# Optimization experiments

Measured on AMD Instinct MI355X. Metric: run time of the kernel, lower is better.

Reference implementation:

```python
import jax, jax.numpy as jnp
import numpy as np

H, NH, NKV, HD, S, B = 4096, 32, 8, 128, 2048, 1
QMAX = 127.0  # int8 symmetric


def fake_quant(x, axis=None):
    """Symmetric int8 fake quantization with straight-through estimator.
    axis=None -> per-tensor dynamic scale; axis=int -> per-channel along that axis."""
    if axis is None:
        amax = jnp.max(jnp.abs(x))
    else:
        amax = jnp.max(jnp.abs(x), axis=axis, keepdims=True)
    scale = jnp.maximum(amax, 1e-8) / QMAX
    q = jnp.clip(jnp.round(x / scale), -QMAX - 1, QMAX) * scale
    return x + jax.lax.stop_gradient(q - x)


def quant_linear(x, w):
    # weight: per-output-channel quant (reduce over in-features axis=1);
    # activation: per-tensor dynamic quant
    xq = fake_quant(x)
    wq = fake_quant(w, axis=1)
    return jnp.einsum('bsh,oh->bso', xq, wq)


def rotate_half(x):
    x1, x2 = jnp.split(x, 2, axis=-1)
    return jnp.concatenate([-x2, x1], axis=-1)


def apply_rope(q, k, cos, sin):
    # q: [B,NH,S,HD], k: [B,NKV,S,HD], cos/sin: [B,S,HD]
    cos = cos[:, None, :, :]
    sin = sin[:, None, :, :]
    return q * cos + rotate_half(q) * sin, k * cos + rotate_half(k) * sin


def setup_inputs() -> dict:
    key = jax.random.key(0)
    ks = jax.random.split(key, 6)
    hidden_states = jax.random.normal(ks[0], (B, S, H), jnp.float32)
    # additive causal mask
    neg = jnp.finfo(jnp.float32).min
    mask = jnp.where(jnp.tril(jnp.ones((S, S), bool)), 0.0, neg)
    attention_mask = jnp.broadcast_to(mask, (B, 1, S, S)).astype(jnp.float32)
    # rotary cos/sin
    inv_freq = 1.0 / (10000.0 ** (jnp.arange(0, HD, 2, dtype=jnp.float32) / HD))
    t = jnp.arange(S, dtype=jnp.float32)
    freqs = jnp.outer(t, inv_freq)                     # [S, HD/2]
    emb = jnp.concatenate([freqs, freqs], axis=-1)     # [S, HD]
    cos = jnp.broadcast_to(jnp.cos(emb), (B, S, HD))
    sin = jnp.broadcast_to(jnp.sin(emb), (B, S, HD))
    sc = 0.02
    wq = jax.random.normal(ks[1], (H, H), jnp.float32) * sc
    wk = jax.random.normal(ks[2], (NKV * HD, H), jnp.float32) * sc
    wv = jax.random.normal(ks[3], (NKV * HD, H), jnp.float32) * sc
    wo = jax.random.normal(ks[4], (H, H), jnp.float32) * sc
    return {"hidden_states": hidden_states, "attention_mask": attention_mask,
            "cos": cos, "sin": sin, "wq": wq, "wk": wk, "wv": wv, "wo": wo}


def reference(hidden_states, attention_mask, cos, sin, wq, wk, wv, wo):
    b, s, _ = hidden_states.shape
    scaling = HD ** -0.5
    q = quant_linear(hidden_states, wq).reshape(b, s, NH, HD).transpose(0, 2, 1, 3)
    k = quant_linear(hidden_states, wk).reshape(b, s, NKV, HD).transpose(0, 2, 1, 3)
    v = quant_linear(hidden_states, wv).reshape(b, s, NKV, HD).transpose(0, 2, 1, 3)
    q, k = apply_rope(q, k, cos, sin)
    groups = NH // NKV
    k = jnp.repeat(k, groups, axis=1)  # [B,NH,S,HD]
    v = jnp.repeat(v, groups, axis=1)
    # quantize before QK^T
    qq = fake_quant(q)
    kq = fake_quant(k)
    attn = jnp.einsum('bhqd,bhkd->bhqk', qq, kq) * scaling
    attn = attn + attention_mask
    attn = jnp.maximum(attn, jnp.finfo(attn.dtype).min)
    attn = jax.nn.softmax(attn.astype(jnp.float32), axis=-1).astype(q.dtype)
    # quantize before PV
    pq = fake_quant(attn)
    vq = fake_quant(v)
    out = jnp.einsum('bhqk,bhkd->bhqd', pq, vq)
    out = out.transpose(0, 2, 1, 3).reshape(b, s, NH * HD)
    out = quant_linear(out, wo)
    return out
```

## Files before the change

kernel.cpp:

```cpp
#include <hip/hip_runtime.h>
#include <cstdint>
#include <cstddef>


#define S_LEN   2048
#define HDIM    4096
#define NHEADS  32
#define NKVH    8
#define HEADD   128
#define QMAXF   127.0f
#define ROPE_BLOCKS 20480

typedef _Float16 half8  __attribute__((ext_vector_type(8)));
typedef float    floatx4 __attribute__((ext_vector_type(4)));

__device__ __forceinline__ float wave_max64(float v){
#pragma unroll
  for (int off = 32; off > 0; off >>= 1) v = fmaxf(v, __shfl_xor(v, off));
  return v;
}
__device__ __forceinline__ float grp16_max(float v){
#pragma unroll
  for (int off = 8; off > 0; off >>= 1) v = fmaxf(v, __shfl_xor(v, off));
  return v;
}
__device__ __forceinline__ float grp16_sum(float v){
#pragma unroll
  for (int off = 8; off > 0; off >>= 1) v += __shfl_xor(v, off);
  return v;
}
__device__ __forceinline__ void atomic_max_f(unsigned* p, float v){
  atomicMax(p, __float_as_uint(v));
}
__device__ __forceinline__ float q8(float x, float scale){
  return fminf(fmaxf(rintf(x / scale), -128.f), 127.f);
}
__device__ __forceinline__ void gload_lds16(const _Float16* g, _Float16* l){
  __builtin_amdgcn_global_load_lds((const __attribute__((address_space(1))) void*)g,
                                   (__attribute__((address_space(3))) void*)l, 16, 0, 0);
}

__device__ __forceinline__ void block_atomic_max(float m, unsigned* out){
  m = wave_max64(m);
  __shared__ float red[4];
  int wid = threadIdx.x >> 6;
  if ((threadIdx.x & 63) == 0) red[wid] = m;
  __syncthreads();
  if (threadIdx.x == 0)
    atomic_max_f(out, fmaxf(fmaxf(red[0], red[1]), fmaxf(red[2], red[3])));
}

__global__ void k_init(float* scal){ if (threadIdx.x < 16) scal[threadIdx.x] = 0.0f; }

__global__ void k_amax(const float* __restrict__ x, size_t n4, unsigned* __restrict__ out){
  size_t i = (size_t)blockIdx.x * blockDim.x + threadIdx.x;
  size_t stride = (size_t)gridDim.x * blockDim.x;
  float m = 0.f;
  for (; i < n4; i += stride){
    float4 v = ((const float4*)x)[i];
    m = fmaxf(m, fmaxf(fmaxf(fabsf(v.x), fabsf(v.y)), fmaxf(fabsf(v.z), fabsf(v.w))));
  }
  block_atomic_max(m, out);
}

__global__ void k_amax_v(const float* __restrict__ Y, unsigned* __restrict__ out){
  size_t i = (size_t)blockIdx.x * blockDim.x + threadIdx.x;
  size_t stride = (size_t)gridDim.x * blockDim.x;
  float m = 0.f;
  for (size_t e = i; e < (size_t)S_LEN * 1024; e += stride){
    size_t s = e >> 10; int c = (int)(e & 1023);
    m = fmaxf(m, fabsf(Y[s * 6144 + 5120 + c]));
  }
  block_atomic_max(m, out);
}

__global__ void k_quant(const float* __restrict__ x, _Float16* __restrict__ q,
                        size_t n4, const float* __restrict__ amax){
  float scale = fmaxf(*amax, 1e-8f) / QMAXF;
  size_t i = (size_t)blockIdx.x * blockDim.x + threadIdx.x;
  size_t stride = (size_t)gridDim.x * blockDim.x;
  for (; i < n4; i += stride){
    float4 v = ((const float4*)x)[i];
    union { _Float16 h[4]; uint2 u; } pk;
    pk.h[0] = (_Float16)q8(v.x, scale);
    pk.h[1] = (_Float16)q8(v.y, scale);
    pk.h[2] = (_Float16)q8(v.z, scale);
    pk.h[3] = (_Float16)q8(v.w, scale);
    ((uint2*)q)[i] = pk.u;
  }
}

__global__ __launch_bounds__(256) void k_quant_w(
    const float* __restrict__ wq, const float* __restrict__ wk,
    const float* __restrict__ wv, const float* __restrict__ wo,
    _Float16* __restrict__ Wall, _Float16* __restrict__ Wo,
    float* __restrict__ wsc)
{
  int row = blockIdx.x;
  const float* src; _Float16* dst;
  if (row < 4096)      { src = wq + (size_t)row * HDIM;          dst = Wall + (size_t)row * HDIM; }
  else if (row < 5120) { src = wk + (size_t)(row - 4096) * HDIM; dst = Wall + (size_t)row * HDIM; }
  else if (row < 6144) { src = wv + (size_t)(row - 5120) * HDIM; dst = Wall + (size_t)row * HDIM; }
  else                 { src = wo + (size_t)(row - 6144) * HDIM; dst = Wo + (size_t)(row - 6144) * HDIM; }
  float4 v[4]; float m = 0.f;
#pragma unroll
  for (int i = 0; i < 4; i++){
    v[i] = ((const float4*)src)[threadIdx.x + i * 256];
    m = fmaxf(m, fmaxf(fmaxf(fabsf(v[i].x), fabsf(v[i].y)), fmaxf(fabsf(v[i].z), fabsf(v[i].w))));
  }
  m = wave_max64(m);
  __shared__ float red[4];
  int wid = threadIdx.x >> 6;
  if ((threadIdx.x & 63) == 0) red[wid] = m;
  __syncthreads();
  float am = fmaxf(fmaxf(red[0], red[1]), fmaxf(red[2], red[3]));
  float scale = fmaxf(am, 1e-8f) / QMAXF;
  if (threadIdx.x == 0) wsc[row] = scale;
#pragma unroll
  for (int i = 0; i < 4; i++){
    union { _Float16 h[4]; uint2 u; } pk;
    pk.h[0] = (_Float16)q8(v[i].x, scale);
    pk.h[1] = (_Float16)q8(v[i].y, scale);
    pk.h[2] = (_Float16)q8(v[i].z, scale);
    pk.h[3] = (_Float16)q8(v[i].w, scale);
    ((uint2*)dst)[threadIdx.x + i * 256] = pk.u;
  }
}

__global__ __launch_bounds__(256) void k_rope(
    float* __restrict__ Y, const float* __restrict__ cosb,
    const float* __restrict__ sinb,
    float* __restrict__ qpart, float* __restrict__ kpart)
{
  int idx = blockIdx.x * 256 + threadIdx.x;
  int s = idx / (40 * 64);
  int rem = idx - s * 40 * 64;
  int head = rem >> 6;
  int d = rem & 63;
  size_t base = (size_t)s * 6144 + (head < 32 ? head * 128 : 4096 + (head - 32) * 128);
  float x1 = Y[base + d], x2 = Y[base + d + 64];
  float c1 = cosb[s * 128 + d],      s1 = sinb[s * 128 + d];
  float c2 = cosb[s * 128 + d + 64], s2 = sinb[s * 128 + d + 64];
  float o1 = x1 * c1 - x2 * s1;
  float o2 = x2 * c2 + x1 * s2;
  Y[base + d] = o1; Y[base + d + 64] = o2;
  float m = wave_max64(fmaxf(fabsf(o1), fabsf(o2)));
  __shared__ float wmax[4]; __shared__ int wisq[4];
  int wid = threadIdx.x >> 6;
  if ((threadIdx.x & 63) == 0){ wmax[wid] = m; wisq[wid] = (head < 32); }
  __syncthreads();
  if (threadIdx.x == 0){
    float qm = 0.f, km = 0.f;
#pragma unroll
    for (int w = 0; w < 4; w++){
      if (wisq[w]) qm = fmaxf(qm, wmax[w]); else km = fmaxf(km, wmax[w]);
    }
    qpart[blockIdx.x] = qm; kpart[blockIdx.x] = km;
  }
}

__global__ __launch_bounds__(256) void k_reduce_qk(
    const float* __restrict__ qpart, const float* __restrict__ kpart,
    float* __restrict__ scal)
{
  const float* src = blockIdx.x ? kpart : qpart;
  float m = 0.f;
  for (int i = threadIdx.x; i < ROPE_BLOCKS; i += 256) m = fmaxf(m, src[i]);
  m = wave_max64(m);
  __shared__ float red[4];
  int wid = threadIdx.x >> 6;
  if ((threadIdx.x & 63) == 0) red[wid] = m;
  __syncthreads();
  if (threadIdx.x == 0)
    scal[1 + blockIdx.x] = fmaxf(fmaxf(red[0], red[1]), fmaxf(red[2], red[3]));
}

__global__ __launch_bounds__(256) void k_quant_qk(
    const float* __restrict__ Y, _Float16* __restrict__ Qh,
    _Float16* __restrict__ Kh, const float* __restrict__ scal)
{
  int i = blockIdx.x * 256 + threadIdx.x;
  int s = i / 1280, c4 = i - s * 1280;
  int col = c4 * 4;
  float4 v = *(const float4*)(Y + (size_t)s * 6144 + col);
  float scale = fmaxf(col < 4096 ? scal[1] : scal[2], 1e-8f) / QMAXF;
  union { _Float16 h[4]; uint2 u; } pk;
  pk.h[0] = (_Float16)q8(v.x, scale);
  pk.h[1] = (_Float16)q8(v.y, scale);
  pk.h[2] = (_Float16)q8(v.z, scale);
  pk.h[3] = (_Float16)q8(v.w, scale);
  if (col < 4096) *(uint2*)(Qh + (size_t)s * 4096 + col) = pk.u;
  else            *(uint2*)(Kh + (size_t)s * 1024 + (col - 4096)) = pk.u;
}

__global__ __launch_bounds__(256) void k_quant_vt(
    const float* __restrict__ Y, _Float16* __restrict__ Vt,
    const float* __restrict__ scal)
{
  __shared__ _Float16 sT[64][72];
  const int s0 = blockIdx.x * 64, kvh = blockIdx.y, dh = blockIdx.z;
  const float scale = fmaxf(scal[3], 1e-8f) / QMAXF;
  const int d = threadIdx.x & 63, srow = threadIdx.x >> 6;
#pragma unroll
  for (int i = 0; i < 16; i++){
    int s = srow + i * 4;
    float v = Y[(size_t)(s0 + s) * 6144 + 5120 + kvh * 128 + dh * 64 + d];
    sT[d][s] = (_Float16)q8(v, scale);
  }
  __syncthreads();
  const int dr = threadIdx.x >> 2, j = threadIdx.x & 3;
  _Float16* dst = Vt + (size_t)kvh * HEADD * S_LEN + (size_t)(dh * 64 + dr) * S_LEN + s0 + j * 16;
  *(uint4*)(dst)     = *(const uint4*)(&sT[dr][j * 16]);
  *(uint4*)(dst + 8) = *(const uint4*)(&sT[dr][j * 16 + 8]);
}

__global__ __launch_bounds__(256) void k_gemm_nt(
    const _Float16* __restrict__ A, const _Float16* __restrict__ B,
    const float* __restrict__ amax_a, const float* __restrict__ sb,
    float* __restrict__ C, int M, int N, int K)
{
  __shared__ _Float16 sA[128 * 32];
  __shared__ _Float16 sB[128 * 32];
  const int m0 = blockIdx.x * 128;
  const int n0 = blockIdx.y * 128;
  const int tid = threadIdx.x;
  const int w = tid >> 6, lane = tid & 63;
  const int quad = lane >> 4, l16 = lane & 15;
  const int wm = (w & 1) * 64, wn = (w >> 1) * 64;
  floatx4 acc[4][4] = {};
  const int srow = w * 16 + (lane >> 2);
  const int scol = (lane & 3) * 8;
  const _Float16* gA0 = A + (size_t)(m0 + srow) * K + scol;
  const _Float16* gA1 = A + (size_t)(m0 + 64 + srow) * K + scol;
  const _Float16* gB0 = B + (size_t)(n0 + srow) * K + scol;
  const _Float16* gB1 = B + (size_t)(n0 + 64 + srow) * K + scol;
  _Float16* dA0 = sA + w * 512 + lane * 8;
  _Float16* dA1 = sA + 2048 + w * 512 + lane * 8;
  _Float16* dB0 = sB + w * 512 + lane * 8;
  _Float16* dB1 = sB + 2048 + w * 512 + lane * 8;

  for (int k0 = 0; k0 < K; k0 += 32){
    __syncthreads();
    gload_lds16(gA0 + k0, dA0);
    gload_lds16(gA1 + k0, dA1);
    gload_lds16(gB0 + k0, dB0);
    gload_lds16(gB1 + k0, dB1);
    __syncthreads();
    half8 af[4], bf[4];
#pragma unroll
    for (int i = 0; i < 4; i++){
      af[i] = *(const half8*)(sA + (wm + i * 16 + l16) * 32 + quad * 8);
      bf[i] = *(const half8*)(sB + (wn + i * 16 + l16) * 32 + quad * 8);
    }
#pragma unroll
    for (int i = 0; i < 4; i++)
#pragma unroll
      for (int j = 0; j < 4; j++)
        acc[i][j] = __builtin_amdgcn_mfma_f32_16x16x32_f16(af[i], bf[j], acc[i][j], 0, 0, 0);
  }
  const float sa = fmaxf(*amax_a, 1e-8f) / QMAXF;
#pragma unroll
  for (int i = 0; i < 4; i++){
    int row = m0 + wm + i * 16 + quad * 4;
#pragma unroll
    for (int j = 0; j < 4; j++){
      int col = n0 + wn + j * 16 + l16;
      float sc2 = sa * sb[col];
#pragma unroll
      for (int rr = 0; rr < 4; rr++)
        C[(size_t)(row + rr) * N + col] = acc[i][j][rr] * sc2;
    }
  }
}

__global__ __launch_bounds__(256, 2) void k_attn(
    const _Float16* __restrict__ Qh,
    const _Float16* __restrict__ Kh,
    const _Float16* __restrict__ Vt,
    const float* __restrict__ scal,
    float* __restrict__ AO)
{
  const int jj = blockIdx.y >> 3;
  const int aa = (jj & 2) ? (int)((blockIdx.x + 16) & 31) : (int)blockIdx.x;
  const int qb = (jj & 1) ? (31 - aa) : aa;
  const int h   = blockIdx.y;
  const int kvh = h >> 2;
  const int tid = threadIdx.x;
  const int wid = tid >> 6, lane = tid & 63;
  const int quad = lane >> 4, l16 = lane & 15;

  __shared__ _Float16 sKV[2][8192];
  __shared__ _Float16 sP[4][1024];

  const float s_q = fmaxf(scal[1], 1e-8f) / QMAXF;
  const float s_k = fmaxf(scal[2], 1e-8f) / QMAXF;
  const float s_v = fmaxf(scal[3], 1e-8f) / QMAXF;
  const float qkscale = s_q * s_k * 0.08838834764831845f;
  const float osc = s_v * (1.0f / QMAXF);

  const int srow7 = (wid * 4 + quad) & 7;
  const int sch   = (l16 & 8) | ((l16 ^ srow7) & 7);
  const _Float16* gKs = Kh + (size_t)(wid * 4 + quad) * 1024 + (size_t)kvh * 128 + sch * 8;
  const int vrg = lane >> 3, vp = lane & 7;
  const _Float16* gVs = Vt + (size_t)kvh * (HEADD * S_LEN)
                           + (size_t)(wid * 8 + vrg) * S_LEN + ((vp ^ vrg) & 7) * 8;

  int krd[4];
#pragma unroll
  for (int kk = 0; kk < 4; kk++){
    int c = kk * 4 + quad;
    krd[kk] = l16 * 128 + ((c & 8) | ((c ^ (l16 & 7)) & 7)) * 8;
  }
  const int vrd0 = l16 * 64 + ((quad       ^ (l16 & 7)) & 7) * 8;
  const int vrd1 = l16 * 64 + (((quad ^ 4) ^ (l16 & 7)) & 7) * 8;

  const int qrow = qb * 64 + wid * 16 + l16;
  half8 qf[4];
#pragma unroll
  for (int kk = 0; kk < 4; kk++)
    qf[kk] = *(const half8*)(Qh + (size_t)qrow * 4096 + h * 128 + kk * 32 + quad * 8);
  const int q_of_reg = qb * 64 + wid * 16 + quad * 4;

  float mrow[4], lrow[4];
#pragma unroll
  for (int rr = 0; rr < 4; rr++){ mrow[rr] = -__builtin_inff(); lrow[rr] = 0.f; }

  auto stage_k = [&](int kt, _Float16* buf){
    const _Float16* g = gKs + (size_t)kt * 65536;
    _Float16* d = buf + wid * 512;
    gload_lds16(g,          d);
    gload_lds16(g + 16384,  d + 2048);
    gload_lds16(g + 32768,  d + 4096);
    gload_lds16(g + 49152,  d + 6144);
  };
  auto stage_v = [&](int kt, _Float16* buf){
    const _Float16* g = gVs + (size_t)kt * 64;
    _Float16* d = buf + wid * 512;
    gload_lds16(g,          d);
    gload_lds16(g + 65536,  d + 2048);
    gload_lds16(g + 131072, d + 4096);
    gload_lds16(g + 196608, d + 6144);
  };

  stage_k(0, sKV[0]);
  __syncthreads();

  for (int kt = 0; kt <= qb; ++kt){
    if (kt < qb) stage_k(kt + 1, sKV[(kt + 1) & 1]);
    const _Float16* kb = sKV[kt & 1];
    float sv[4][4];
    const bool diag = (kt == qb);
    __builtin_amdgcn_s_setprio(1);
#pragma unroll
    for (int nt = 0; nt < 4; nt++){
      floatx4 c = {};
#pragma unroll
      for (int kk = 0; kk < 4; kk++){
        half8 bf = *(const half8*)(kb + nt * 2048 + krd[kk]);
        c = __builtin_amdgcn_mfma_f32_16x16x32_f16(qf[kk], bf, c, 0, 0, 0);
      }
      if (diag){
        int kpos = kt * 64 + nt * 16 + l16;
#pragma unroll
        for (int rr = 0; rr < 4; rr++)
          sv[nt][rr] = (kpos <= q_of_reg + rr) ? c[rr] * qkscale : -__builtin_inff();
      } else {
#pragma unroll
        for (int rr = 0; rr < 4; rr++) sv[nt][rr] = c[rr] * qkscale;
      }
    }
    __builtin_amdgcn_s_setprio(0);
#pragma unroll
    for (int rr = 0; rr < 4; rr++){
      float lmax = fmaxf(fmaxf(sv[0][rr], sv[1][rr]), fmaxf(sv[2][rr], sv[3][rr]));
      float tmax = grp16_max(lmax);
      float mnew = fmaxf(mrow[rr], tmax);
      float lsum = 0.f;
#pragma unroll
      for (int nt = 0; nt < 4; nt++) lsum += __expf(sv[nt][rr] - mnew);
      lsum = grp16_sum(lsum);
      lrow[rr] = lrow[rr] * __expf(mrow[rr] - mnew) + lsum;
      mrow[rr] = mnew;
    }
    __syncthreads();
  }

  float il[4];
#pragma unroll
  for (int rr = 0; rr < 4; rr++) il[rr] = QMAXF * __builtin_amdgcn_rcpf(lrow[rr]);

  floatx4 accO[8] = {};
  _Float16* sKb = sKV[0];
  _Float16* sVb = sKV[1];
  _Float16* sPw = sP[wid];

  for (int kt = 0; kt <= qb; ++kt){
    __syncthreads();
    stage_k(kt, sKb);
    stage_v(kt, sVb);
    __syncthreads();
    const bool diag = (kt == qb);
    __builtin_amdgcn_s_setprio(1);
#pragma unroll
    for (int nt = 0; nt < 4; nt++){
      floatx4 c = {};
#pragma unroll
      for (int kk = 0; kk < 4; kk++){
        half8 bf = *(const half8*)(sKb + nt * 2048 + krd[kk]);
        c = __builtin_amdgcn_mfma_f32_16x16x32_f16(qf[kk], bf, c, 0, 0, 0);
      }
      int kpos = kt * 64 + nt * 16 + l16;
#pragma unroll
      for (int rr = 0; rr < 4; rr++){
        float pq = fminf(rintf(__expf(c[rr] * qkscale - mrow[rr]) * il[rr]), 127.f);
        if (diag && kpos > q_of_reg + rr) pq = 0.f;
        int row = quad * 4 + rr;
        sPw[row * 64 + ((nt * 2 + (l16 >> 3)) ^ (row & 7)) * 8 + (l16 & 7)] = (_Float16)pq;
      }
    }
    __builtin_amdgcn_s_setprio(0);
    half8 pf0 = *(const half8*)(sPw + vrd0);
    half8 pf1 = *(const half8*)(sPw + vrd1);
    __builtin_amdgcn_s_setprio(1);
#pragma unroll
    for (int dt = 0; dt < 8; dt++){
      half8 b0 = *(const half8*)(sVb + dt * 1024 + vrd0);
      half8 b1 = *(const half8*)(sVb + dt * 1024 + vrd1);
      accO[dt] = __builtin_amdgcn_mfma_f32_16x16x32_f16(pf0, b0, accO[dt], 0, 0, 0);
      accO[dt] = __builtin_amdgcn_mfma_f32_16x16x32_f16(pf1, b1, accO[dt], 0, 0, 0);
    }
    __builtin_amdgcn_s_setprio(0);
  }

#pragma unroll
  for (int dt = 0; dt < 8; dt++){
    int col = h * 128 + dt * 16 + l16;
#pragma unroll
    for (int rr = 0; rr < 4; rr++)
      AO[(size_t)(q_of_reg + rr) * 4096 + col] = accO[dt][rr] * osc;
  }
}

extern "C" void kernel_launch(void* const* d_in, const int* in_sizes, int n_in,
                              void* d_out, int out_size, void* d_ws, size_t ws_size,
                              hipStream_t stream)
{
  const float* hidden = (const float*)d_in[0];
  const float* cosb = (const float*)d_in[2];
  const float* sinb = (const float*)d_in[3];
  const float* wq = (const float*)d_in[4];
  const float* wk = (const float*)d_in[5];
  const float* wv = (const float*)d_in[6];
  const float* wo = (const float*)d_in[7];
  float* out = (float*)d_out;

  char* ws = (char*)d_ws;
  size_t off = 0;
  auto alloc = [&](size_t bytes){ size_t o = off; off += (bytes + 255) & ~(size_t)255; return o; };
  float*    scal  = (float*)   (ws + alloc(64));
  float*    wsc   = (float*)   (ws + alloc(10240 * 4));
  float*    qpart = (float*)   (ws + alloc(ROPE_BLOCKS * 4));
  float*    kpart = (float*)   (ws + alloc(ROPE_BLOCKS * 4));
  _Float16* Wall  = (_Float16*)(ws + alloc((size_t)6144 * 4096 * 2));
  _Float16* Wo    = (_Float16*)(ws + alloc((size_t)4096 * 4096 * 2));
  _Float16* Xq    = (_Float16*)(ws + alloc((size_t)2048 * 4096 * 2));
  float*    Y     = (float*)   (ws + alloc((size_t)2048 * 6144 * 4));
  _Float16* Qh  = Xq;
  _Float16* Kh  = Wall;
  _Float16* Vt  = Wall + (size_t)2048 * 1024;
  float*    AO  = Y;
  _Float16* AOq = (_Float16*)((char*)Y + (size_t)2048 * 4096 * 4);

  unsigned* su = (unsigned*)scal;

  k_init<<<dim3(1), dim3(64), 0, stream>>>(scal);
  k_quant_w<<<dim3(10240), dim3(256), 0, stream>>>(wq, wk, wv, wo, Wall, Wo, wsc);
  k_amax<<<dim3(256), dim3(256), 0, stream>>>(hidden, (size_t)(2048 * 4096 / 4), su + 0);
  k_quant<<<dim3(2048), dim3(256), 0, stream>>>(hidden, Xq, (size_t)(2048 * 4096 / 4), scal + 0);
  k_gemm_nt<<<dim3(16, 48), dim3(256), 0, stream>>>(Xq, Wall, scal + 0, wsc, Y, 2048, 6144, 4096);
  k_rope<<<dim3(ROPE_BLOCKS), dim3(256), 0, stream>>>(Y, cosb, sinb, qpart, kpart);
  k_reduce_qk<<<dim3(2), dim3(256), 0, stream>>>(qpart, kpart, scal);
  k_amax_v<<<dim3(256), dim3(256), 0, stream>>>(Y, su + 3);
  k_quant_qk<<<dim3(10240), dim3(256), 0, stream>>>(Y, Qh, Kh, scal);
  k_quant_vt<<<dim3(32, 8, 2), dim3(256), 0, stream>>>(Y, Vt, scal);
  k_attn<<<dim3(32, 32), dim3(256), 0, stream>>>(Qh, Kh, Vt, scal, AO);
  k_amax<<<dim3(256), dim3(256), 0, stream>>>(AO, (size_t)(2048 * 4096 / 4), su + 4);
  k_quant<<<dim3(2048), dim3(256), 0, stream>>>(AO, AOq, (size_t)(2048 * 4096 / 4), scal + 4);
  k_gemm_nt<<<dim3(16, 32), dim3(256), 0, stream>>>(AOq, Wo, scal + 4, wsc + 6144, out, 2048, 4096, 4096);
}
```

Before: 679.9 us.

## Restructure attention kernel: paired causal blocks, transposed QK, register P, pipelined KV

The attention kernel now has each block process two complementary query tiles (pair and 31-pair), which balances causal work across 512 blocks instead of remapping 1024 blocks. QK^T is computed transposed (K as the A operand) so each lane owns a single query row and softmax reductions need only two cross-quad shuffles. The quantized P tile is packed to fp16 in registers and redistributed by wave shuffles instead of going through LDS. The PV pass now double-buffers K and V with prefetch of the next tile. The trade-offs are fewer blocks, and therefore less parallelism, plus more shuffle instructions and twice the LDS for the separate K and V buffers.

```diff
diff --git a/kernel.cpp b/kernel.cpp
--- a/kernel.cpp
+++ b/kernel.cpp
@@ -12,6 +12,7 @@
 #define ROPE_BLOCKS 20480
 
 typedef _Float16 half8  __attribute__((ext_vector_type(8)));
+typedef _Float16 half2v __attribute__((ext_vector_type(2)));
 typedef float    floatx4 __attribute__((ext_vector_type(4)));
 
 __device__ __forceinline__ float wave_max64(float v){
@@ -19,14 +20,14 @@
   for (int off = 32; off > 0; off >>= 1) v = fmaxf(v, __shfl_xor(v, off));
   return v;
 }
-__device__ __forceinline__ float grp16_max(float v){
-#pragma unroll
-  for (int off = 8; off > 0; off >>= 1) v = fmaxf(v, __shfl_xor(v, off));
+__device__ __forceinline__ float quad_max(float v){
+  v = fmaxf(v, __shfl_xor(v, 16));
+  v = fmaxf(v, __shfl_xor(v, 32));
   return v;
 }
-__device__ __forceinline__ float grp16_sum(float v){
-#pragma unroll
-  for (int off = 8; off > 0; off >>= 1) v += __shfl_xor(v, off);
+__device__ __forceinline__ float quad_sum(float v){
+  v += __shfl_xor(v, 16);
+  v += __shfl_xor(v, 32);
   return v;
 }
 __device__ __forceinline__ void atomic_max_f(unsigned* p, float v){
@@ -280,17 +281,15 @@
     const float* __restrict__ scal,
     float* __restrict__ AO)
 {
-  const int jj = blockIdx.y >> 3;
-  const int aa = (jj & 2) ? (int)((blockIdx.x + 16) & 31) : (int)blockIdx.x;
-  const int qb = (jj & 1) ? (31 - aa) : aa;
-  const int h   = blockIdx.y;
-  const int kvh = h >> 2;
-  const int tid = threadIdx.x;
-  const int wid = tid >> 6, lane = tid & 63;
+  const int pair = blockIdx.x;
+  const int h    = blockIdx.y;
+  const int kvh  = h >> 2;
+  const int tid  = threadIdx.x;
+  const int wid  = tid >> 6, lane = tid & 63;
   const int quad = lane >> 4, l16 = lane & 15;
 
-  __shared__ _Float16 sKV[2][8192];
-  __shared__ _Float16 sP[4][1024];
+  __shared__ _Float16 sK[2][8192];
+  __shared__ _Float16 sV[2][8192];
 
   const float s_q = fmaxf(scal[1], 1e-8f) / QMAXF;
   const float s_k = fmaxf(scal[2], 1e-8f) / QMAXF;
@@ -314,130 +313,152 @@
   const int vrd0 = l16 * 64 + ((quad       ^ (l16 & 7)) & 7) * 8;
   const int vrd1 = l16 * 64 + (((quad ^ 4) ^ (l16 & 7)) & 7) * 8;
 
-  const int qrow = qb * 64 + wid * 16 + l16;
-  half8 qf[4];
-#pragma unroll
-  for (int kk = 0; kk < 4; kk++)
-    qf[kk] = *(const half8*)(Qh + (size_t)qrow * 4096 + h * 128 + kk * 32 + quad * 8);
-  const int q_of_reg = qb * 64 + wid * 16 + quad * 4;
-
-  float mrow[4], lrow[4];
-#pragma unroll
-  for (int rr = 0; rr < 4; rr++){ mrow[rr] = -__builtin_inff(); lrow[rr] = 0.f; }
-
-  auto stage_k = [&](int kt, _Float16* buf){
+  const int sl0 = l16 + 32 * (quad & 1);
+  const int sl1 = sl0 + 16;
+
+  auto stage_k = [&](int kt, int buf){
     const _Float16* g = gKs + (size_t)kt * 65536;
-    _Float16* d = buf + wid * 512;
+    _Float16* d = sK[buf] + wid * 512;
     gload_lds16(g,          d);
     gload_lds16(g + 16384,  d + 2048);
     gload_lds16(g + 32768,  d + 4096);
     gload_lds16(g + 49152,  d + 6144);
   };
-  auto stage_v = [&](int kt, _Float16* buf){
+  auto stage_v = [&](int kt, int buf){
     const _Float16* g = gVs + (size_t)kt * 64;
-    _Float16* d = buf + wid * 512;
+    _Float16* d = sV[buf] + wid * 512;
     gload_lds16(g,          d);
     gload_lds16(g + 65536,  d + 2048);
     gload_lds16(g + 131072, d + 4096);
     gload_lds16(g + 196608, d + 6144);
   };
 
-  stage_k(0, sKV[0]);
-  __syncthreads();
-
-  for (int kt = 0; kt <= qb; ++kt){
-    if (kt < qb) stage_k(kt + 1, sKV[(kt + 1) & 1]);
-    const _Float16* kb = sKV[kt & 1];
-    float sv[4][4];
-    const bool diag = (kt == qb);
-    __builtin_amdgcn_s_setprio(1);
-#pragma unroll
-    for (int nt = 0; nt < 4; nt++){
-      floatx4 c = {};
-#pragma unroll
-      for (int kk = 0; kk < 4; kk++){
-        half8 bf = *(const half8*)(kb + nt * 2048 + krd[kk]);
-        c = __builtin_amdgcn_mfma_f32_16x16x32_f16(qf[kk], bf, c, 0, 0, 0);
+  for (int half = 0; half < 2; half++){
+    const int qb = half ? (31 - pair) : pair;
+    const int ql = qb * 64 + wid * 16 + l16;
+    half8 qf[4];
+#pragma unroll
+    for (int kk = 0; kk < 4; kk++)
+      qf[kk] = *(const half8*)(Qh + (size_t)ql * 4096 + h * 128 + kk * 32 + quad * 8);
+
+    float m = -__builtin_inff(), l = 0.f;
+
+    stage_k(0, 0);
+    __syncthreads();
+    for (int kt = 0; kt <= qb; ++kt){
+      if (kt < qb) stage_k(kt + 1, (kt + 1) & 1);
+      const _Float16* kb = sK[kt & 1];
+      const bool diag = (kt == qb);
+      float s[4][4];
+      __builtin_amdgcn_s_setprio(1);
+#pragma unroll
+      for (int nt = 0; nt < 4; nt++){
+        floatx4 c = {};
+#pragma unroll
+        for (int kk = 0; kk < 4; kk++){
+          half8 kf = *(const half8*)(kb + nt * 2048 + krd[kk]);
+          c = __builtin_amdgcn_mfma_f32_16x16x32_f16(kf, qf[kk], c, 0, 0, 0);
+        }
+#pragma unroll
+        for (int rr = 0; rr < 4; rr++){
+          int kpos = kt * 64 + nt * 16 + quad * 4 + rr;
+          float v = c[rr] * qkscale;
+          s[nt][rr] = (diag && kpos > ql) ? -__builtin_inff() : v;
+        }
       }
-      if (diag){
-        int kpos = kt * 64 + nt * 16 + l16;
-#pragma unroll
-        for (int rr = 0; rr < 4; rr++)
-          sv[nt][rr] = (kpos <= q_of_reg + rr) ? c[rr] * qkscale : -__builtin_inff();
-      } else {
-#pragma unroll
-        for (int rr = 0; rr < 4; rr++) sv[nt][rr] = c[rr] * qkscale;
+      __builtin_amdgcn_s_setprio(0);
+      float tm = s[0][0];
+#pragma unroll
+      for (int nt = 0; nt < 4; nt++)
+#pragma unroll
+        for (int rr = 0; rr < 4; rr++) tm = fmaxf(tm, s[nt][rr]);
+      tm = quad_max(tm);
+      float mnew = fmaxf(m, tm);
+      float ls = 0.f;
+#pragma unroll
+      for (int nt = 0; nt < 4; nt++)
+#pragma unroll
+        for (int rr = 0; rr < 4; rr++) ls += __expf(s[nt][rr] - mnew);
+      ls = quad_sum(ls);
+      l = l * __expf(m - mnew) + ls;
+      m = mnew;
+      __syncthreads();
+    }
+    const float il = QMAXF * __builtin_amdgcn_rcpf(l);
+
+    floatx4 accO[8] = {};
+    stage_k(0, 0); stage_v(0, 0);
+    __syncthreads();
+    for (int kt = 0; kt <= qb; ++kt){
+      if (kt < qb){ stage_k(kt + 1, (kt + 1) & 1); stage_v(kt + 1, (kt + 1) & 1); }
+      const _Float16* kb = sK[kt & 1];
+      const _Float16* vb = sV[kt & 1];
+      const bool diag = (kt == qb);
+      float p[4][4];
+      __builtin_amdgcn_s_setprio(1);
+#pragma unroll
+      for (int nt = 0; nt < 4; nt++){
+        floatx4 c = {};
+#pragma unroll
+        for (int kk = 0; kk < 4; kk++){
+          half8 kf = *(const half8*)(kb + nt * 2048 + krd[kk]);
+          c = __builtin_amdgcn_mfma_f32_16x16x32_f16(kf, qf[kk], c, 0, 0, 0);
+        }
+#pragma unroll
+        for (int rr = 0; rr < 4; rr++) p[nt][rr] = c[rr];
       }
+      __builtin_amdgcn_s_setprio(0);
+      unsigned ph[4][2];
+#pragma unroll
+      for (int nt = 0; nt < 4; nt++){
+        float pq[4];
+#pragma unroll
+        for (int rr = 0; rr < 4; rr++){
+          int kpos = kt * 64 + nt * 16 + quad * 4 + rr;
+          float v = fminf(rintf(__expf(p[nt][rr] * qkscale - m) * il), 127.f);
+          pq[rr] = (diag && kpos > ql) ? 0.f : v;
+        }
+        ph[nt][0] = __builtin_bit_cast(unsigned, __builtin_amdgcn_cvt_pkrtz(pq[0], pq[1]));
+        ph[nt][1] = __builtin_bit_cast(unsigned, __builtin_amdgcn_cvt_pkrtz(pq[2], pq[3]));
+      }
+      half8 pb[2];
+      const bool hi = (quad >= 2);
+#pragma unroll
+      for (int ks = 0; ks < 2; ks++){
+        unsigned wa0 = __shfl((int)ph[2 * ks][0],     sl0);
+        unsigned wb0 = __shfl((int)ph[2 * ks + 1][0], sl0);
+        unsigned wa1 = __shfl((int)ph[2 * ks][1],     sl0);
+        unsigned wb1 = __shfl((int)ph[2 * ks + 1][1], sl0);
+        unsigned wa2 = __shfl((int)ph[2 * ks][0],     sl1);
+        unsigned wb2 = __shfl((int)ph[2 * ks + 1][0], sl1);
+        unsigned wa3 = __shfl((int)ph[2 * ks][1],     sl1);
+        unsigned wb3 = __shfl((int)ph[2 * ks + 1][1], sl1);
+        union { unsigned w[4]; half8 v; } u;
+        u.w[0] = hi ? wb0 : wa0;
+        u.w[1] = hi ? wb1 : wa1;
+        u.w[2] = hi ? wb2 : wa2;
+        u.w[3] = hi ? wb3 : wa3;
+        pb[ks] = u.v;
+      }
+      __builtin_amdgcn_s_setprio(1);
+#pragma unroll
+      for (int dt = 0; dt < 8; dt++){
+        half8 v0 = *(const half8*)(vb + dt * 1024 + vrd0);
+        half8 v1 = *(const half8*)(vb + dt * 1024 + vrd1);
+        accO[dt] = __builtin_amdgcn_mfma_f32_16x16x32_f16(v0, pb[0], accO[dt], 0, 0, 0);
+        accO[dt] = __builtin_amdgcn_mfma_f32_16x16x32_f16(v1, pb[1], accO[dt], 0, 0, 0);
+      }
+      __builtin_amdgcn_s_setprio(0);
+      __syncthreads();
     }
-    __builtin_amdgcn_s_setprio(0);
-#pragma unroll
-    for (int rr = 0; rr < 4; rr++){
-      float lmax = fmaxf(fmaxf(sv[0][rr], sv[1][rr]), fmaxf(sv[2][rr], sv[3][rr]));
-      float tmax = grp16_max(lmax);
-      float mnew = fmaxf(mrow[rr], tmax);
-      float lsum = 0.f;
-#pragma unroll
-      for (int nt = 0; nt < 4; nt++) lsum += __expf(sv[nt][rr] - mnew);
-      lsum = grp16_sum(lsum);
-      lrow[rr] = lrow[rr] * __expf(mrow[rr] - mnew) + lsum;
-      mrow[rr] = mnew;
+
+#pragma unroll
+    for (int dt = 0; dt < 8; dt++){
+      float4 o;
+      o.x = accO[dt][0] * osc; o.y = accO[dt][1] * osc;
+      o.z = accO[dt][2] * osc; o.w = accO[dt][3] * osc;
+      *(float4*)(AO + (size_t)ql * 4096 + h * 128 + dt * 16 + quad * 4) = o;
     }
-    __syncthreads();
-  }
-
-  float il[4];
-#pragma unroll
-  for (int rr = 0; rr < 4; rr++) il[rr] = QMAXF * __builtin_amdgcn_rcpf(lrow[rr]);
-
-  floatx4 accO[8] = {};
-  _Float16* sKb = sKV[0];
-  _Float16* sVb = sKV[1];
-  _Float16* sPw = sP[wid];
-
-  for (int kt = 0; kt <= qb; ++kt){
-    __syncthreads();
-    stage_k(kt, sKb);
-    stage_v(kt, sVb);
-    __syncthreads();
-    const bool diag = (kt == qb);
-    __builtin_amdgcn_s_setprio(1);
-#pragma unroll
-    for (int nt = 0; nt < 4; nt++){
-      floatx4 c = {};
-#pragma unroll
-      for (int kk = 0; kk < 4; kk++){
-        half8 bf = *(const half8*)(sKb + nt * 2048 + krd[kk]);
-        c = __builtin_amdgcn_mfma_f32_16x16x32_f16(qf[kk], bf, c, 0, 0, 0);
-      }
-      int kpos = kt * 64 + nt * 16 + l16;
-#pragma unroll
-      for (int rr = 0; rr < 4; rr++){
-        float pq = fminf(rintf(__expf(c[rr] * qkscale - mrow[rr]) * il[rr]), 127.f);
-        if (diag && kpos > q_of_reg + rr) pq = 0.f;
-        int row = quad * 4 + rr;
-        sPw[row * 64 + ((nt * 2 + (l16 >> 3)) ^ (row & 7)) * 8 + (l16 & 7)] = (_Float16)pq;
-      }
-    }
-    __builtin_amdgcn_s_setprio(0);
-    half8 pf0 = *(const half8*)(sPw + vrd0);
-    half8 pf1 = *(const half8*)(sPw + vrd1);
-    __builtin_amdgcn_s_setprio(1);
-#pragma unroll
-    for (int dt = 0; dt < 8; dt++){
-      half8 b0 = *(const half8*)(sVb + dt * 1024 + vrd0);
-      half8 b1 = *(const half8*)(sVb + dt * 1024 + vrd1);
-      accO[dt] = __builtin_amdgcn_mfma_f32_16x16x32_f16(pf0, b0, accO[dt], 0, 0, 0);
-      accO[dt] = __builtin_amdgcn_mfma_f32_16x16x32_f16(pf1, b1, accO[dt], 0, 0, 0);
-    }
-    __builtin_amdgcn_s_setprio(0);
-  }
-
-#pragma unroll
-  for (int dt = 0; dt < 8; dt++){
-    int col = h * 128 + dt * 16 + l16;
-#pragma unroll
-    for (int rr = 0; rr < 4; rr++)
-      AO[(size_t)(q_of_reg + rr) * 4096 + col] = accO[dt][rr] * osc;
   }
 }
 
@@ -483,7 +504,7 @@
   k_amax_v<<<dim3(256), dim3(256), 0, stream>>>(Y, su + 3);
   k_quant_qk<<<dim3(10240), dim3(256), 0, stream>>>(Y, Qh, Kh, scal);
   k_quant_vt<<<dim3(32, 8, 2), dim3(256), 0, stream>>>(Y, Vt, scal);
-  k_attn<<<dim3(32, 32), dim3(256), 0, stream>>>(Qh, Kh, Vt, scal, AO);
+  k_attn<<<dim3(16, 32), dim3(256), 0, stream>>>(Qh, Kh, Vt, scal, AO);
   k_amax<<<dim3(256), dim3(256), 0, stream>>>(AO, (size_t)(2048 * 4096 / 4), su + 4);
   k_quant<<<dim3(2048), dim3(256), 0, stream>>>(AO, AOq, (size_t)(2048 * 4096 / 4), scal + 4);
   k_gemm_nt<<<dim3(16, 32), dim3(256), 0, stream>>>(AOq, Wo, scal + 4, wsc + 6144, out, 2048, 4096, 4096);
```

After: 651.8 us. 1.04x faster.
